# Kernel tuning notes

Hardware: AMD Instinct MI355X
Metric: run time of the kernel (lower is better)

Reference implementation:

```python
import jax, jax.numpy as jnp
import numpy as np

H = 16          # num_attention_heads
HD = 64         # hidden_size_per_attention_head
EPS = 1e-12

def _layernorm(x, w, b):
    u = x.mean(-1, keepdims=True)
    s = ((x - u) ** 2).mean(-1, keepdims=True)
    return w * (x - u) / jnp.sqrt(s + EPS) + b

def _split_heads(x):
    b, s, d = x.shape
    return x.reshape(b, s, H, d // H).transpose(0, 2, 1, 3)  # [b,h,s,hd]

def _merge_heads(x):
    b, h, s, hd = x.shape
    return x.transpose(0, 2, 1, 3).reshape(b, s, h * hd)


def setup_inputs() -> dict:
    key = jax.random.key(0)
    ks = jax.random.split(key, 20)
    B, S, T, D, F = 4, 1024, 1024, 1024, 4096
    w = lambda k, shp: (jax.random.normal(k, shp, jnp.float32) * 0.02)
    return {
        "hidden_states": jax.random.normal(ks[0], (B, S, D), jnp.float32),
        "enc_hidden_states": jax.random.normal(ks[1], (B, T, D), jnp.float32),
        "enc_attn_mask": jnp.zeros((B, 1, 1, T), jnp.float32),
        "dec_attn_mask": jnp.tril(jnp.ones((S, S), jnp.float32)).reshape(1, 1, S, S),
        "ln1_w": jnp.ones((D,), jnp.float32), "ln1_b": jnp.zeros((D,), jnp.float32),
        "qkv_w": w(ks[2], (D, 3 * D)), "qkv_b": jnp.zeros((3 * D,), jnp.float32),
        "attn_o_w": w(ks[3], (D, D)), "attn_o_b": jnp.zeros((D,), jnp.float32),
        "ln2_w": jnp.ones((D,), jnp.float32), "ln2_b": jnp.zeros((D,), jnp.float32),
        "q_w": w(ks[4], (D, D)), "q_b": jnp.zeros((D,), jnp.float32),
        "kv_w": w(ks[5], (D, 2 * D)), "kv_b": jnp.zeros((2 * D,), jnp.float32),
        "ca_o_w": w(ks[6], (D, D)), "ca_o_b": jnp.zeros((D,), jnp.float32),
        "ln3_w": jnp.ones((D,), jnp.float32), "ln3_b": jnp.zeros((D,), jnp.float32),
        "ffn_in_w": w(ks[7], (D, F)), "ffn_in_b": jnp.zeros((F,), jnp.float32),
        "ffn_out_w": w(ks[8], (F, D)), "ffn_out_b": jnp.zeros((D,), jnp.float32),
    }


def reference(hidden_states, enc_hidden_states, enc_attn_mask, dec_attn_mask,
              ln1_w, ln1_b, qkv_w, qkv_b, attn_o_w, attn_o_b,
              ln2_w, ln2_b, q_w, q_b, kv_w, kv_b, ca_o_w, ca_o_b,
              ln3_w, ln3_b, ffn_in_w, ffn_in_b, ffn_out_w, ffn_out_b):
    scale = 1.0 / jnp.sqrt(jnp.float32(HD))
    # dropout layers are identity (eval mode)

    # ---- self-attention (ltor multiplicative mask formula) ----
    residual = hidden_states
    x = _layernorm(hidden_states, ln1_w, ln1_b)
    qkv = x @ qkv_w + qkv_b
    q, k, v = jnp.split(qkv, 3, axis=-1)
    q, k, v = _split_heads(q), _split_heads(k), _split_heads(v)
    scores = jnp.einsum('bhsd,bhtd->bhst', q, k) * scale
    scores = scores * dec_attn_mask - 10000.0 * (1.0 - dec_attn_mask)
    probs = jax.nn.softmax(scores, axis=-1)
    ctx = _merge_heads(jnp.einsum('bhst,bhtd->bhsd', probs, v))
    hidden_states = residual + (ctx @ attn_o_w + attn_o_b)

    # ---- cross-attention (additive enc mask) ----
    residual = hidden_states
    x = _layernorm(hidden_states, ln2_w, ln2_b)
    q = _split_heads(x @ q_w + q_b)
    kv = enc_hidden_states @ kv_w + kv_b
    k, v = jnp.split(kv, 2, axis=-1)
    k, v = _split_heads(k), _split_heads(v)
    scores = jnp.einsum('bhsd,bhtd->bhst', q, k) * scale + enc_attn_mask
    probs = jax.nn.softmax(scores, axis=-1)
    ctx = _merge_heads(jnp.einsum('bhst,bhtd->bhsd', probs, v))
    hidden_states = residual + (ctx @ ca_o_w + ca_o_b)

    # ---- FFN ----
    residual = hidden_states
    x = _layernorm(hidden_states, ln3_w, ln3_b)
    x = jax.nn.gelu(x @ ffn_in_w + ffn_in_b, approximate=False)
    x = x @ ffn_out_w + ffn_out_b
    return residual + x
```

## Files before the change

kernel.cpp:

```cpp
#include <hip/hip_runtime.h>
#include <cstdint>
#include <cstddef>

typedef unsigned short u16;
typedef __bf16 bf16x8 __attribute__((ext_vector_type(8)));
typedef float f32x4 __attribute__((ext_vector_type(4)));

__device__ __forceinline__ u16 f2bf(float f) {
  unsigned u = __float_as_uint(f);
  u += 0x7fffu + ((u >> 16) & 1u);
  return (u16)(u >> 16);
}

__device__ __forceinline__ float block_sum(float v, float* sbuf, int tid) {
#pragma unroll
  for (int off = 1; off < 64; off <<= 1) v += __shfl_xor(v, off, 64);
  if ((tid & 63) == 0) sbuf[tid >> 6] = v;
  __syncthreads();
  v = sbuf[0] + sbuf[1] + sbuf[2] + sbuf[3];
  __syncthreads();
  return v;
}

__device__ __forceinline__ void gld16(const void* g, void* l) {
  __builtin_amdgcn_global_load_lds((const __attribute__((address_space(1))) void*)g,
                                   (__attribute__((address_space(3))) void*)l,
                                   16, 0, 0);
}

__device__ __forceinline__ void swz(int& bx, int& by) {
  const int gx = gridDim.x, gy = gridDim.y;
  const int id = blockIdx.y * gx + blockIdx.x;
  const int xcd = id & 7, slot = id >> 3;
  bx = xcd * (gx >> 3) + slot / gy;
  by = slot % gy;
}


#define GEMM_BODY(Aptr, Bptr, Kdim)                                              \
  const int lane = tid & 63, wave = tid >> 6;                                    \
  const int l15 = lane & 15, g = (lane >> 4) & 3;                                \
  const int wm = (wave >> 1) * 64, wn = (wave & 1) * 64;                         \
  const int c0 = tid, c1 = tid + 256;                                            \
  const int ar0 = c0 >> 2, ak0 = (c0 & 3) * 8;                                   \
  const int ar1 = c1 >> 2, ak1 = (c1 & 3) * 8;                                   \
  const size_t aoff0 = (size_t)(m0 + ar0) * Kdim + ak0;                          \
  const size_t aoff1 = (size_t)(m0 + ar1) * Kdim + ak1;                          \
  const size_t boff0 = (size_t)(n0 + ar0) * Kdim + ak0;                          \
  const size_t boff1 = (size_t)(n0 + ar1) * Kdim + ak1;                          \
  f32x4 acc[4][4] = {};                                                          \
  for (int k0 = kstart; k0 < kend; k0 += 32) {                                   \
    gld16(Aptr + aoff0 + k0, As + (size_t)c0 * 8);                               \
    gld16(Aptr + aoff1 + k0, As + (size_t)c1 * 8);                               \
    gld16(Bptr + boff0 + k0, Bs + (size_t)c0 * 8);                               \
    gld16(Bptr + boff1 + k0, Bs + (size_t)c1 * 8);                               \
    __syncthreads();                                                             \
    bf16x8 af[4], bg[4];                                                         \
    _Pragma("unroll")                                                            \
    for (int i = 0; i < 4; i++) {                                                \
      af[i] = *(const bf16x8*)(As + (wm + i * 16 + l15) * 32 + g * 8);           \
      bg[i] = *(const bf16x8*)(Bs + (wn + i * 16 + l15) * 32 + g * 8);           \
    }                                                                            \
    _Pragma("unroll")                                                            \
    for (int i = 0; i < 4; i++)                                                  \
      _Pragma("unroll")                                                          \
      for (int j = 0; j < 4; j++)                                                \
        acc[i][j] = __builtin_amdgcn_mfma_f32_16x16x32_bf16(af[i], bg[j], acc[i][j], 0, 0, 0); \
    __syncthreads();                                                             \
  }

__global__ __launch_bounds__(256) void gemm_gelu(
    const u16* __restrict__ A, const u16* __restrict__ B,
    const float* __restrict__ bias, u16* __restrict__ out, int N, int K)
{
  __shared__ __align__(16) u16 As[128 * 32];
  __shared__ __align__(16) u16 Bs[128 * 32];
  const int tid = threadIdx.x;
  int bx, by; swz(bx, by);
  const int m0 = by * 128, n0 = bx * 128;
  const int kstart = 0, kend = K;
  GEMM_BODY(A, B, K)

#pragma unroll
  for (int i = 0; i < 4; i++) {
#pragma unroll
    for (int j = 0; j < 4; j++) {
      const int col = n0 + wn + j * 16 + l15;
#pragma unroll
      for (int r = 0; r < 4; r++) {
        const int gm = m0 + wm + i * 16 + g * 4 + r;
        float v = acc[i][j][r] + bias[col];
        v = 0.5f * v * (1.0f + erff(v * 0.70710678118654752f));
        out[(size_t)gm * N + col] = f2bf(v);
      }
    }
  }
}

__global__ __launch_bounds__(256) void gemm_qkv(
    const u16* __restrict__ A, const u16* __restrict__ B,
    const float* __restrict__ bias,
    u16* __restrict__ qh, u16* __restrict__ kt, u16* __restrict__ vt,
    int K, int mode)
{
  __shared__ __align__(16) u16 As[128 * 32];
  __shared__ __align__(16) u16 Bs[128 * 32];
  const int tid = threadIdx.x;
  int bx, by; swz(bx, by);
  const int m0 = by * 128, n0 = bx * 128;
  const int kstart = 0, kend = K;
  GEMM_BODY(A, B, K)

#pragma unroll
  for (int i = 0; i < 4; i++) {
#pragma unroll
    for (int j = 0; j < 4; j++) {
      const int col = n0 + wn + j * 16 + l15;
      const int sec = (n0 + wn + j * 16) >> 10;
      const int tgt = (mode == 1) ? sec : sec + 1;
#pragma unroll
      for (int r = 0; r < 4; r++) {
        const int gm = m0 + wm + i * 16 + g * 4 + r;
        const float v = acc[i][j][r] + bias[col];
        const int cl = col & 1023, h = cl >> 6, d = cl & 63;
        const int z = (gm >> 10) * 16 + h, s = gm & 1023;
        if (tgt == 0)
          qh[((size_t)z * 1024 + s) * 64 + d] = f2bf(v * 0.125f);
        else if (tgt == 1)
          kt[((((size_t)z * 8 + (s >> 7)) * 8 + (d >> 3)) * 128 + (s & 127)) * 8 + (d & 7)] = f2bf(v);
        else
          vt[((size_t)z * 8 + (s >> 7)) * 8192 + (((s >> 3) & 15) * 64 + d) * 8 + (s & 7)] = f2bf(v);
      }
    }
  }
}

__global__ __launch_bounds__(256) void gemm_splitk(
    const u16* __restrict__ A, const u16* __restrict__ B,
    float* __restrict__ part, int K, int Klen)
{
  __shared__ __align__(16) u16 As[128 * 32];
  __shared__ __align__(16) u16 Bs[128 * 32];
  const int tid = threadIdx.x;
  int bx, by; swz(bx, by);
  const int m0 = by * 128, n0 = bx * 128;
  const int kstart = blockIdx.z * Klen, kend = kstart + Klen;
  float* outP = part + (size_t)blockIdx.z * (4096ULL * 1024);
  GEMM_BODY(A, B, K)

#pragma unroll
  for (int i = 0; i < 4; i++)
#pragma unroll
    for (int j = 0; j < 4; j++) {
      const int col = n0 + wn + j * 16 + l15;
#pragma unroll
      for (int r = 0; r < 4; r++) {
        const int gm = m0 + wm + i * 16 + g * 4 + r;
        outP[(size_t)gm * 1024 + col] = acc[i][j][r];
      }
    }
}

__global__ __launch_bounds__(256, 2) void flash_attn(
    const u16* __restrict__ qh, const u16* __restrict__ kt, const u16* __restrict__ vt,
    const float* __restrict__ emask, u16* __restrict__ ctx, int causal)
{
  __shared__ __align__(16) u16 sK[8192];
  __shared__ __align__(16) u16 sV[8192];
  __shared__ __align__(16) u16 sP[128 * 72];

  const int tid = threadIdx.x, lane = tid & 63, wave = tid >> 6;
  const int l15 = lane & 15, g = (lane >> 4) & 3;
  const int id = blockIdx.y * 8 + blockIdx.x;
  const int xcd = id & 7, slot = id >> 3;
  const int z = xcd * 8 + (slot >> 3), b = z >> 4, h = z & 15;
  const int m0 = (slot & 7) * 128;
  const int r0 = wave * 32;

  bf16x8 qf[2][2];
  {
    const u16* qz = qh + ((size_t)z * 1024 + m0 + r0 + l15) * 64 + g * 8;
#pragma unroll
    for (int i2 = 0; i2 < 2; ++i2)
#pragma unroll
      for (int kc = 0; kc < 2; ++kc)
        qf[i2][kc] = *(const bf16x8*)(qz + (size_t)i2 * 16 * 64 + kc * 32);
  }

  float m_i[2][4], l_i[2][4];
#pragma unroll
  for (int i2 = 0; i2 < 2; ++i2)
#pragma unroll
    for (int r = 0; r < 4; ++r) { m_i[i2][r] = -1.0e30f; l_i[i2][r] = 0.0f; }

  f32x4 o[2][4] = {};
  const int tmax = causal ? m0 : 896;

  for (int t0 = 0; t0 <= tmax; t0 += 128) {
    const u16* ktile = kt + ((size_t)z * 8 + (t0 >> 7)) * 8192;
    const u16* vtile = vt + ((size_t)z * 8 + (t0 >> 7)) * 8192;
    __syncthreads();
#pragma unroll
    for (int i = 0; i < 4; ++i) {
      const int off = (wave * 4 + i) * 512 + lane * 8;
      gld16(ktile + off, sK + off);
      gld16(vtile + off, sV + off);
    }
    __syncthreads();

#pragma unroll
    for (int ci = 0; ci < 2; ++ci) {
      if (causal && t0 == m0 && ci * 64 > r0 + 31) continue;

      f32x4 sa[2][4] = {};
#pragma unroll
      for (int kc = 0; kc < 2; ++kc) {
        bf16x8 bg[4];
#pragma unroll
        for (int jn = 0; jn < 4; ++jn)
          bg[jn] = *(const bf16x8*)(sK + ((kc * 4 + g) * 128 + ci * 64 + jn * 16 + l15) * 8);
#pragma unroll
        for (int i2 = 0; i2 < 2; ++i2)
#pragma unroll
          for (int jn = 0; jn < 4; ++jn)
            sa[i2][jn] = __builtin_amdgcn_mfma_f32_16x16x32_bf16(qf[i2][kc], bg[jn], sa[i2][jn], 0, 0, 0);
      }

      if (causal) {
        if (t0 == m0 && ci * 64 + 63 > r0) {
#pragma unroll
          for (int i2 = 0; i2 < 2; ++i2)
#pragma unroll
            for (int jn = 0; jn < 4; ++jn) {
              const int col = ci * 64 + jn * 16 + l15;
#pragma unroll
              for (int r = 0; r < 4; ++r) {
                const int row = r0 + i2 * 16 + g * 4 + r;
                if (col > row) sa[i2][jn][r] = -3.0e38f;
              }
            }
        }
      } else {
#pragma unroll
        for (int jn = 0; jn < 4; ++jn) {
          const float mv = emask[(size_t)b * 1024 + t0 + ci * 64 + jn * 16 + l15];
#pragma unroll
          for (int i2 = 0; i2 < 2; ++i2)
#pragma unroll
            for (int r = 0; r < 4; ++r) sa[i2][jn][r] += mv;
        }
      }

      float alpha[2][4];
#pragma unroll
      for (int i2 = 0; i2 < 2; ++i2)
#pragma unroll
        for (int r = 0; r < 4; ++r) {
          const int rowl = r0 + i2 * 16 + g * 4 + r;
          float v = fmaxf(fmaxf(sa[i2][0][r], sa[i2][1][r]), fmaxf(sa[i2][2][r], sa[i2][3][r]));
          v = fmaxf(v, __shfl_xor(v, 1, 64));
          v = fmaxf(v, __shfl_xor(v, 2, 64));
          v = fmaxf(v, __shfl_xor(v, 4, 64));
          v = fmaxf(v, __shfl_xor(v, 8, 64));
          const float mo = m_i[i2][r];
          const float mn = fmaxf(mo, v);
          m_i[i2][r] = mn;
          alpha[i2][r] = __expf(mo - mn);
          float s = 0.0f;
#pragma unroll
          for (int jn = 0; jn < 4; ++jn) {
            const float p = __expf(sa[i2][jn][r] - mn);
            s += p;
            sP[rowl * 72 + jn * 16 + l15] = f2bf(p);
          }
          s += __shfl_xor(s, 1, 64);
          s += __shfl_xor(s, 2, 64);
          s += __shfl_xor(s, 4, 64);
          s += __shfl_xor(s, 8, 64);
          l_i[i2][r] = alpha[i2][r] * l_i[i2][r] + s;
        }

#pragma unroll
      for (int i2 = 0; i2 < 2; ++i2)
#pragma unroll
        for (int jn = 0; jn < 4; ++jn)
#pragma unroll
          for (int r = 0; r < 4; ++r)
            o[i2][jn][r] *= alpha[i2][r];

      asm volatile("s_waitcnt lgkmcnt(0)" ::: "memory");
#pragma unroll
      for (int kc2 = 0; kc2 < 2; ++kc2) {
        bf16x8 pa[2], vb[4];
#pragma unroll
        for (int i2 = 0; i2 < 2; ++i2)
          pa[i2] = *(const bf16x8*)(sP + (r0 + i2 * 16 + l15) * 72 + kc2 * 32 + g * 8);
#pragma unroll
        for (int jn = 0; jn < 4; ++jn)
          vb[jn] = *(const bf16x8*)(sV + ((ci * 8 + kc2 * 4 + g) * 64 + jn * 16 + l15) * 8);
#pragma unroll
        for (int i2 = 0; i2 < 2; ++i2)
#pragma unroll
          for (int jn = 0; jn < 4; ++jn)
            o[i2][jn] = __builtin_amdgcn_mfma_f32_16x16x32_bf16(pa[i2], vb[jn], o[i2][jn], 0, 0, 0);
      }
    }
  }

#pragma unroll
  for (int i2 = 0; i2 < 2; ++i2)
#pragma unroll
    for (int r = 0; r < 4; ++r) {
      const float inv = 1.0f / l_i[i2][r];
      const size_t base = ((size_t)(b * 1024 + m0 + r0 + i2 * 16 + g * 4 + r)) * 1024 + h * 64;
#pragma unroll
      for (int jn = 0; jn < 4; ++jn)
        ctx[base + jn * 16 + l15] = f2bf(o[i2][jn][r] * inv);
    }
}

struct PrepArgs {
  const float* w[7]; u16* wt[7]; int K[7]; int N[7]; int cum[7];
  const float* enc; u16* enc_bf;
  const float* hid; const float* ln1w; const float* ln1b; u16* xln;
};
__global__ __launch_bounds__(256) void prep_kernel(PrepArgs a) {
  __shared__ float t[32][33];
  __shared__ float sbuf[4];
  const int bb = blockIdx.x, tid = threadIdx.x;
  if (bb < 16384) {
    int wi = 0;
#pragma unroll
    for (int i = 0; i < 7; ++i) if (bb >= a.cum[i]) wi = i + 1; else break;
    const int base = wi ? a.cum[wi - 1] : 0;
    const int tileIdx = bb - base;
    const int Kd = a.K[wi], Nd = a.N[wi], nx = Nd >> 5;
    const int n0 = (tileIdx % nx) * 32, k0 = (tileIdx / nx) * 32;
    const float* w = a.w[wi]; u16* wt = a.wt[wi];
    const int tx = tid & 31, ty = tid >> 5;
#pragma unroll
    for (int r = ty; r < 32; r += 8) t[r][tx] = w[(size_t)(k0 + r) * Nd + n0 + tx];
    __syncthreads();
#pragma unroll
    for (int r = ty; r < 32; r += 8) wt[(size_t)(n0 + r) * Kd + k0 + tx] = f2bf(t[tx][r]);
  } else if (bb < 20480) {
    const size_t i = ((size_t)(bb - 16384) * 256 + tid) * 4;
    const float4 v = *(const float4*)(a.enc + i);
    ushort4 o; o.x = f2bf(v.x); o.y = f2bf(v.y); o.z = f2bf(v.z); o.w = f2bf(v.w);
    *(ushort4*)(a.enc_bf + i) = o;
  } else {
    const int row = bb - 20480;
    const float4 v = *(const float4*)(a.hid + (size_t)row * 1024 + tid * 4);
    float s = block_sum(v.x + v.y + v.z + v.w, sbuf, tid);
    const float u = s * (1.0f / 1024.0f);
    const float d0 = v.x - u, d1 = v.y - u, d2 = v.z - u, d3 = v.w - u;
    float sq = block_sum(d0 * d0 + d1 * d1 + d2 * d2 + d3 * d3, sbuf, tid);
    const float rstd = rsqrtf(sq * (1.0f / 1024.0f) + 1e-12f);
    const int c = tid * 4;
    ushort4 o;
    o.x = f2bf(a.ln1w[c + 0] * d0 * rstd + a.ln1b[c + 0]);
    o.y = f2bf(a.ln1w[c + 1] * d1 * rstd + a.ln1b[c + 1]);
    o.z = f2bf(a.ln1w[c + 2] * d2 * rstd + a.ln1b[c + 2]);
    o.w = f2bf(a.ln1w[c + 3] * d3 * rstd + a.ln1b[c + 3]);
    *(ushort4*)(a.xln + (size_t)row * 1024 + c) = o;
  }
}

__global__ __launch_bounds__(256) void ln_red_kernel(
    const float* __restrict__ p0, const float* __restrict__ p1,
    const float* __restrict__ bias, const float* __restrict__ res,
    const float* __restrict__ w, const float* __restrict__ b,
    float* __restrict__ hOut, u16* __restrict__ xln)
{
  __shared__ float sbuf[4];
  const int row = blockIdx.x, tid = threadIdx.x;
  const size_t off = (size_t)row * 1024 + tid * 4;
  const int c = tid * 4;
  const float4 a0 = *(const float4*)(p0 + off);
  const float4 a1 = *(const float4*)(p1 + off);
  const float4 bs = *(const float4*)(bias + c);
  const float4 rs = *(const float4*)(res + off);
  float4 v;
  v.x = a0.x + a1.x + bs.x + rs.x;
  v.y = a0.y + a1.y + bs.y + rs.y;
  v.z = a0.z + a1.z + bs.z + rs.z;
  v.w = a0.w + a1.w + bs.w + rs.w;
  *(float4*)(hOut + off) = v;
  float s = block_sum(v.x + v.y + v.z + v.w, sbuf, tid);
  const float u = s * (1.0f / 1024.0f);
  const float d0 = v.x - u, d1 = v.y - u, d2 = v.z - u, d3 = v.w - u;
  float sq = block_sum(d0 * d0 + d1 * d1 + d2 * d2 + d3 * d3, sbuf, tid);
  const float rstd = rsqrtf(sq * (1.0f / 1024.0f) + 1e-12f);
  ushort4 o;
  o.x = f2bf(w[c + 0] * d0 * rstd + b[c + 0]);
  o.y = f2bf(w[c + 1] * d1 * rstd + b[c + 1]);
  o.z = f2bf(w[c + 2] * d2 * rstd + b[c + 2]);
  o.w = f2bf(w[c + 3] * d3 * rstd + b[c + 3]);
  *(ushort4*)(xln + off) = o;
}

__global__ __launch_bounds__(256) void reduce_q_kernel(
    const float* __restrict__ p0, const float* __restrict__ p1,
    const float* __restrict__ bias, u16* __restrict__ qh)
{
  const int m = blockIdx.x, tid = threadIdx.x;
  const size_t off = (size_t)m * 1024 + tid * 4;
  const int n = tid * 4, h = n >> 6, d = n & 63;
  const int b = m >> 10, s = m & 1023;
  const float4 a0 = *(const float4*)(p0 + off);
  const float4 a1 = *(const float4*)(p1 + off);
  const float4 bs = *(const float4*)(bias + n);
  ushort4 o;
  o.x = f2bf((a0.x + a1.x + bs.x) * 0.125f);
  o.y = f2bf((a0.y + a1.y + bs.y) * 0.125f);
  o.z = f2bf((a0.z + a1.z + bs.z) * 0.125f);
  o.w = f2bf((a0.w + a1.w + bs.w) * 0.125f);
  *(ushort4*)(qh + ((size_t)((b * 16 + h) * 1024 + s)) * 64 + d) = o;
}

__global__ __launch_bounds__(256) void reduce_out_kernel(
    const float* __restrict__ p0, const float* __restrict__ p1,
    const float* __restrict__ bias, const float* __restrict__ res,
    float* __restrict__ out)
{
  const int m = blockIdx.x, tid = threadIdx.x;
  const size_t off = (size_t)m * 1024 + tid * 4;
  const int c = tid * 4;
  const float4 a0 = *(const float4*)(p0 + off);
  const float4 a1 = *(const float4*)(p1 + off);
  const float4 bs = *(const float4*)(bias + c);
  const float4 rs = *(const float4*)(res + off);
  float4 v;
  v.x = a0.x + a1.x + bs.x + rs.x;
  v.y = a0.y + a1.y + bs.y + rs.y;
  v.z = a0.z + a1.z + bs.z + rs.z;
  v.w = a0.w + a1.w + bs.w + rs.w;
  *(float4*)(out + off) = v;
}

constexpr size_t MB = 1024ULL * 1024;
constexpr size_t WT_QKV    = 0;
constexpr size_t WT_ATTN_O = 6 * MB;
constexpr size_t WT_Q      = 8 * MB;
constexpr size_t WT_KV     = 10 * MB;
constexpr size_t WT_CA_O   = 14 * MB;
constexpr size_t WT_FFN_IN = 16 * MB;
constexpr size_t WT_FFN_OUT= 24 * MB;
constexpr size_t ENC_BF    = 32 * MB;
constexpr size_t XLN       = 40 * MB;
constexpr size_t QH        = 48 * MB;
constexpr size_t KT        = 56 * MB;
constexpr size_t VT        = 64 * MB;
constexpr size_t CTX       = 72 * MB;
constexpr size_t HBUF      = 80 * MB;
constexpr size_t SP0       = 96 * MB;
constexpr size_t SP1       = 112 * MB;
constexpr size_t FFN_MID   = 128 * MB;

extern "C" void kernel_launch(void* const* d_in, const int* in_sizes, int n_in,
                              void* d_out, int out_size, void* d_ws, size_t ws_size,
                              hipStream_t stream) {
  const float* hidden   = (const float*)d_in[0];
  const float* enc      = (const float*)d_in[1];
  const float* encm     = (const float*)d_in[2];
  const float* ln1w = (const float*)d_in[4],  *ln1b = (const float*)d_in[5];
  const float* qkv_w = (const float*)d_in[6], *qkv_b = (const float*)d_in[7];
  const float* attn_o_w = (const float*)d_in[8], *attn_o_b = (const float*)d_in[9];
  const float* ln2w = (const float*)d_in[10], *ln2b = (const float*)d_in[11];
  const float* q_w = (const float*)d_in[12],  *q_b = (const float*)d_in[13];
  const float* kv_w = (const float*)d_in[14], *kv_b = (const float*)d_in[15];
  const float* ca_o_w = (const float*)d_in[16], *ca_o_b = (const float*)d_in[17];
  const float* ln3w = (const float*)d_in[18], *ln3b = (const float*)d_in[19];
  const float* ffn_in_w = (const float*)d_in[20], *ffn_in_b = (const float*)d_in[21];
  const float* ffn_out_w = (const float*)d_in[22], *ffn_out_b = (const float*)d_in[23];

  char* ws = (char*)d_ws;
  u16* wt_qkv    = (u16*)(ws + WT_QKV);
  u16* wt_attn_o = (u16*)(ws + WT_ATTN_O);
  u16* wt_q      = (u16*)(ws + WT_Q);
  u16* wt_kv     = (u16*)(ws + WT_KV);
  u16* wt_ca_o   = (u16*)(ws + WT_CA_O);
  u16* wt_ffn_in = (u16*)(ws + WT_FFN_IN);
  u16* wt_ffn_out= (u16*)(ws + WT_FFN_OUT);
  u16* enc_bf = (u16*)(ws + ENC_BF);
  u16* xln    = (u16*)(ws + XLN);
  u16* qh     = (u16*)(ws + QH);
  u16* kt     = (u16*)(ws + KT);
  u16* vt     = (u16*)(ws + VT);
  u16* ctx    = (u16*)(ws + CTX);
  float* hF   = (float*)(ws + HBUF);
  float* sp0  = (float*)(ws + SP0);
  float* sp1  = (float*)(ws + SP1);
  u16* ffn_mid = (u16*)(ws + FFN_MID);

  PrepArgs pa;
  pa.w[0] = qkv_w;    pa.wt[0] = wt_qkv;     pa.K[0] = 1024; pa.N[0] = 3072; pa.cum[0] = 3072;
  pa.w[1] = attn_o_w; pa.wt[1] = wt_attn_o;  pa.K[1] = 1024; pa.N[1] = 1024; pa.cum[1] = 4096;
  pa.w[2] = q_w;      pa.wt[2] = wt_q;       pa.K[2] = 1024; pa.N[2] = 1024; pa.cum[2] = 5120;
  pa.w[3] = kv_w;     pa.wt[3] = wt_kv;      pa.K[3] = 1024; pa.N[3] = 2048; pa.cum[3] = 7168;
  pa.w[4] = ca_o_w;   pa.wt[4] = wt_ca_o;    pa.K[4] = 1024; pa.N[4] = 1024; pa.cum[4] = 8192;
  pa.w[5] = ffn_in_w; pa.wt[5] = wt_ffn_in;  pa.K[5] = 1024; pa.N[5] = 4096; pa.cum[5] = 12288;
  pa.w[6] = ffn_out_w;pa.wt[6] = wt_ffn_out; pa.K[6] = 4096; pa.N[6] = 1024; pa.cum[6] = 16384;
  pa.enc = enc; pa.enc_bf = enc_bf;
  pa.hid = hidden; pa.ln1w = ln1w; pa.ln1b = ln1b; pa.xln = xln;
  prep_kernel<<<24576, 256, 0, stream>>>(pa);

  gemm_qkv<<<dim3(24, 32), 256, 0, stream>>>(xln, wt_qkv, qkv_b, qh, kt, vt, 1024, 1);
  flash_attn<<<dim3(8, 64), 256, 0, stream>>>(qh, kt, vt, nullptr, ctx, 1);
  gemm_splitk<<<dim3(8, 32, 2), 256, 0, stream>>>(ctx, wt_attn_o, sp0, 1024, 512);
  ln_red_kernel<<<4096, 256, 0, stream>>>(sp0, sp1, attn_o_b, hidden, ln2w, ln2b, hF, xln);

  gemm_splitk<<<dim3(8, 32, 2), 256, 0, stream>>>(xln, wt_q, sp0, 1024, 512);
  reduce_q_kernel<<<4096, 256, 0, stream>>>(sp0, sp1, q_b, qh);
  gemm_qkv<<<dim3(16, 32), 256, 0, stream>>>(enc_bf, wt_kv, kv_b, nullptr, kt, vt, 1024, 3);
  flash_attn<<<dim3(8, 64), 256, 0, stream>>>(qh, kt, vt, encm, ctx, 0);
  gemm_splitk<<<dim3(8, 32, 2), 256, 0, stream>>>(ctx, wt_ca_o, sp0, 1024, 512);
  ln_red_kernel<<<4096, 256, 0, stream>>>(sp0, sp1, ca_o_b, hF, ln3w, ln3b, hF, xln);

  gemm_gelu<<<dim3(32, 32), 256, 0, stream>>>(xln, wt_ffn_in, ffn_in_b, ffn_mid, 4096, 1024);
  gemm_splitk<<<dim3(8, 32, 2), 256, 0, stream>>>(ffn_mid, wt_ffn_out, sp0, 4096, 2048);
  reduce_out_kernel<<<4096, 256, 0, stream>>>(sp0, sp1, ffn_out_b, hF, (float*)d_out);
}
```

Before: 603.0 us.

## Double-buffer LDS tiles in GEMM kernels to overlap global loads with MFMA

Replaces the single-buffered GEMM main loop with a two-stage ping-pong LDS pipeline: the next K-slice is issued via global_load_lds into the alternate buffer before computing on the current one. Synchronisation uses explicit s_waitcnt vmcnt(4) and lgkmcnt plus s_barrier in inline asm. This targets the exposed global-memory latency in every GEMM (QKV, GELU FFN, split-K). It doubles shared memory per block, from 16KB to 32KB, and relies on the hand-written waitcnt values being correct.

After: 599.1 us. Within noise of the previous version (-0.6%).

```diff
diff --git a/kernel.cpp b/kernel.cpp
--- a/kernel.cpp
+++ b/kernel.cpp
@@ -37,7 +37,7 @@
 }
 
 
-#define GEMM_BODY(Aptr, Bptr, Kdim)                                              \
+#define GEMM_SETUP(Kdim)                                                         \
   const int lane = tid & 63, wave = tid >> 6;                                    \
   const int l15 = lane & 15, g = (lane >> 4) & 3;                                \
   const int wm = (wave >> 1) * 64, wn = (wave & 1) * 64;                         \
@@ -47,39 +47,53 @@
   const size_t aoff0 = (size_t)(m0 + ar0) * Kdim + ak0;                          \
   const size_t aoff1 = (size_t)(m0 + ar1) * Kdim + ak1;                          \
   const size_t boff0 = (size_t)(n0 + ar0) * Kdim + ak0;                          \
-  const size_t boff1 = (size_t)(n0 + ar1) * Kdim + ak1;                          \
+  const size_t boff1 = (size_t)(n0 + ar1) * Kdim + ak1;
+
+#define GEMM_STAGE(Aptr, Bptr, kk, buf)                                          \
+    gld16(Aptr + aoff0 + (kk), As + (buf) * 4096 + (size_t)c0 * 8);              \
+    gld16(Aptr + aoff1 + (kk), As + (buf) * 4096 + (size_t)c1 * 8);              \
+    gld16(Bptr + boff0 + (kk), Bs + (buf) * 4096 + (size_t)c0 * 8);              \
+    gld16(Bptr + boff1 + (kk), Bs + (buf) * 4096 + (size_t)c1 * 8);
+
+#define GEMM_COMPUTE(buf)                                                        \
+    { bf16x8 af[4], bg[4];                                                       \
+      _Pragma("unroll")                                                          \
+      for (int i = 0; i < 4; i++) {                                              \
+        af[i] = *(const bf16x8*)(As + (buf) * 4096 + (wm + i * 16 + l15) * 32 + g * 8); \
+        bg[i] = *(const bf16x8*)(Bs + (buf) * 4096 + (wn + i * 16 + l15) * 32 + g * 8); \
+      }                                                                          \
+      _Pragma("unroll")                                                          \
+      for (int i = 0; i < 4; i++)                                                \
+        _Pragma("unroll")                                                        \
+        for (int j = 0; j < 4; j++)                                              \
+          acc[i][j] = __builtin_amdgcn_mfma_f32_16x16x32_bf16(af[i], bg[j], acc[i][j], 0, 0, 0); }
+
+#define GEMM_BODY_DB(Aptr, Bptr, Kdim)                                           \
+  GEMM_SETUP(Kdim)                                                               \
   f32x4 acc[4][4] = {};                                                          \
-  for (int k0 = kstart; k0 < kend; k0 += 32) {                                   \
-    gld16(Aptr + aoff0 + k0, As + (size_t)c0 * 8);                               \
-    gld16(Aptr + aoff1 + k0, As + (size_t)c1 * 8);                               \
-    gld16(Bptr + boff0 + k0, Bs + (size_t)c0 * 8);                               \
-    gld16(Bptr + boff1 + k0, Bs + (size_t)c1 * 8);                               \
-    __syncthreads();                                                             \
-    bf16x8 af[4], bg[4];                                                         \
-    _Pragma("unroll")                                                            \
-    for (int i = 0; i < 4; i++) {                                                \
-      af[i] = *(const bf16x8*)(As + (wm + i * 16 + l15) * 32 + g * 8);           \
-      bg[i] = *(const bf16x8*)(Bs + (wn + i * 16 + l15) * 32 + g * 8);           \
-    }                                                                            \
-    _Pragma("unroll")                                                            \
-    for (int i = 0; i < 4; i++)                                                  \
-      _Pragma("unroll")                                                          \
-      for (int j = 0; j < 4; j++)                                                \
-        acc[i][j] = __builtin_amdgcn_mfma_f32_16x16x32_bf16(af[i], bg[j], acc[i][j], 0, 0, 0); \
-    __syncthreads();                                                             \
-  }
+  GEMM_STAGE(Aptr, Bptr, kstart, 0)                                              \
+  int cur = 0;                                                                   \
+  for (int k0 = kstart; k0 + 32 < kend; k0 += 32) {                              \
+    GEMM_STAGE(Aptr, Bptr, k0 + 32, cur ^ 1)                                     \
+    asm volatile("s_waitcnt vmcnt(4)\ns_barrier" ::: "memory");                  \
+    GEMM_COMPUTE(cur)                                                            \
+    asm volatile("s_waitcnt lgkmcnt(0)\ns_barrier" ::: "memory");                \
+    cur ^= 1;                                                                    \
+  }                                                                              \
+  asm volatile("s_waitcnt vmcnt(0)\ns_barrier" ::: "memory");                    \
+  GEMM_COMPUTE(cur)
 
 __global__ __launch_bounds__(256) void gemm_gelu(
     const u16* __restrict__ A, const u16* __restrict__ B,
     const float* __restrict__ bias, u16* __restrict__ out, int N, int K)
 {
-  __shared__ __align__(16) u16 As[128 * 32];
-  __shared__ __align__(16) u16 Bs[128 * 32];
+  __shared__ __align__(16) u16 As[2 * 128 * 32];
+  __shared__ __align__(16) u16 Bs[2 * 128 * 32];
   const int tid = threadIdx.x;
   int bx, by; swz(bx, by);
   const int m0 = by * 128, n0 = bx * 128;
   const int kstart = 0, kend = K;
-  GEMM_BODY(A, B, K)
+  GEMM_BODY_DB(A, B, K)
 
 #pragma unroll
   for (int i = 0; i < 4; i++) {
@@ -103,13 +117,13 @@
     u16* __restrict__ qh, u16* __restrict__ kt, u16* __restrict__ vt,
     int K, int mode)
 {
-  __shared__ __align__(16) u16 As[128 * 32];
-  __shared__ __align__(16) u16 Bs[128 * 32];
+  __shared__ __align__(16) u16 As[2 * 128 * 32];
+  __shared__ __align__(16) u16 Bs[2 * 128 * 32];
   const int tid = threadIdx.x;
   int bx, by; swz(bx, by);
   const int m0 = by * 128, n0 = bx * 128;
   const int kstart = 0, kend = K;
-  GEMM_BODY(A, B, K)
+  GEMM_BODY_DB(A, B, K)
 
 #pragma unroll
   for (int i = 0; i < 4; i++) {
@@ -139,14 +153,14 @@
     const u16* __restrict__ A, const u16* __restrict__ B,
     float* __restrict__ part, int K, int Klen)
 {
-  __shared__ __align__(16) u16 As[128 * 32];
-  __shared__ __align__(16) u16 Bs[128 * 32];
+  __shared__ __align__(16) u16 As[2 * 128 * 32];
+  __shared__ __align__(16) u16 Bs[2 * 128 * 32];
   const int tid = threadIdx.x;
   int bx, by; swz(bx, by);
   const int m0 = by * 128, n0 = bx * 128;
   const int kstart = blockIdx.z * Klen, kend = kstart + Klen;
   float* outP = part + (size_t)blockIdx.z * (4096ULL * 1024);
-  GEMM_BODY(A, B, K)
+  GEMM_BODY_DB(A, B, K)
 
 #pragma unroll
   for (int i = 0; i < 4; i++)
```
